# Kernel tuning notes

Hardware: AMD Instinct MI355X
Metric: run time of the kernel (lower is better)

Reference implementation:

```python
import jax, jax.numpy as jnp
import numpy as np

DIMS = [2048, 1024, 512, 256, 128, 64, 32, 16, 8, 4, 2]
IN_CH = [3, 8, 32, 64, 64, 64, 128, 256, 512, 512, 512]
FEAT = [8, 32, 64, 64, 64, 128, 256, 512, 512, 512, 1024]
B = 512
K = 16


def setup_inputs() -> dict:
    key = jax.random.key(0)
    keys = jax.random.split(key, 64)
    inp = {"x": jax.random.normal(keys[0], (B, 3, 2048), dtype=jnp.float32)}
    for i, d in enumerate(DIMS):
        inp[f"c{i}"] = jax.random.randint(keys[1 + i], (d,), 0, 3, dtype=jnp.int64)
    for i in range(11):
        cin, f = IN_CH[i], FEAT[i]
        inp[f"W{i+1}"] = jax.random.normal(keys[20 + 2 * i], (3 * f, cin), dtype=jnp.float32) / jnp.sqrt(jnp.float32(cin))
        inp[f"b{i+1}"] = jnp.zeros((3 * f,), dtype=jnp.float32)
    inp["Wfc"] = jax.random.normal(keys[60], (K, 1024), dtype=jnp.float32) / jnp.sqrt(jnp.float32(1024))
    inp["bfc"] = jnp.zeros((K,), dtype=jnp.float32)
    return inp


def _kdconv(x, W, b, sel, featdim, dim):
    # pointwise conv (kernel size 1) + relu: [B, in, dim] -> [B, 3*featdim, dim]
    y = jax.nn.relu(jnp.einsum('oi,bid->bod', W, x) + b[None, :, None])
    bsz = y.shape[0]
    # faithful to torch: view [B, featdim, 3*dim], then gather index d*3 + sel[d]
    y = y.reshape(bsz, featdim, 3 * dim)
    idx = sel + 3 * jnp.arange(dim, dtype=sel.dtype)
    y = jnp.take(y, idx, axis=2)                       # [B, featdim, dim]
    y = y.reshape(bsz, featdim, dim // 2, 2)
    return jnp.max(y, axis=-1)                          # [B, featdim, dim//2]


def reference(x, c0, c1, c2, c3, c4, c5, c6, c7, c8, c9, c10,
              W1, b1, W2, b2, W3, b3, W4, b4, W5, b5, W6, b6,
              W7, b7, W8, b8, W9, b9, W10, b10, W11, b11, Wfc, bfc):
    cs = [c0, c1, c2, c3, c4, c5, c6, c7, c8, c9, c10]
    Ws = [W1, W2, W3, W4, W5, W6, W7, W8, W9, W10, W11]
    bs = [b1, b2, b3, b4, b5, b6, b7, b8, b9, b10, b11]
    y = x
    for i in range(11):
        y = _kdconv(y, Ws[i], bs[i], cs[i], FEAT[i], DIMS[i])
    y = y.reshape(-1, 1024)
    logits = y @ Wfc.T + bfc
    return jax.nn.log_softmax(logits, axis=1)
```

## Files before the change

kernel.cpp:

```cpp
#include <hip/hip_runtime.h>
#include <cstdint>
#include <cmath>


typedef __attribute__((ext_vector_type(8))) short bhalf8;
typedef __attribute__((ext_vector_type(4))) float floatx4;

__device__ __forceinline__ unsigned short f2bf(float f) {
    uint32_t u = __float_as_uint(f);
    u += 0x7FFFu + ((u >> 16) & 1u);
    return (unsigned short)(u >> 16);
}
__device__ __forceinline__ float bf2f(unsigned short u) {
    return __uint_as_float(((uint32_t)u) << 16);
}

struct WPrep {
    const float* src[9];
    unsigned short* dst[9];
    int n4[9];
    int csh[4];
    int sm[4];
};

__global__ __launch_bounds__(256)
void l01_kernel(const float* __restrict__ x,
                const float* __restrict__ W0, const float* __restrict__ b0,
                const int* __restrict__ sel0,
                const float* __restrict__ W1, const float* __restrict__ b1,
                const int* __restrict__ sel1,
                unsigned short* __restrict__ out,
                WPrep wp, int nL1) {
    const int tid = threadIdx.x;

    if ((int)blockIdx.x >= nL1) {
        const int stride = (gridDim.x - nL1) * 256;
        const int g0 = (blockIdx.x - nL1) * 256 + tid;
        #pragma unroll
        for (int l = 0; l < 4; ++l) {
            const float4* s = reinterpret_cast<const float4*>(wp.src[l]);
            char* dbase = (char*)wp.dst[l];
            const int n16 = wp.n4[l] >> 1;
            const int csh = wp.csh[l], sm = wp.sm[l];
            for (int i = g0; i < n16; i += stride) {
                const float4 va = s[2 * i], vb = s[2 * i + 1];
                uint4 o;
                o.x = (uint32_t)f2bf(va.x) | ((uint32_t)f2bf(va.y) << 16);
                o.y = (uint32_t)f2bf(va.z) | ((uint32_t)f2bf(va.w) << 16);
                o.z = (uint32_t)f2bf(vb.x) | ((uint32_t)f2bf(vb.y) << 16);
                o.w = (uint32_t)f2bf(vb.z) | ((uint32_t)f2bf(vb.w) << 16);
                const int row = i >> csh;
                const int c   = i - (row << csh);
                *(uint4*)(dbase + (row << (csh + 4)) +
                          ((c * 16) ^ ((row & sm) << 4))) = o;
            }
        }
        #pragma unroll
        for (int l = 4; l < 9; ++l) {
            const float4* s = reinterpret_cast<const float4*>(wp.src[l]);
            uint2* d = reinterpret_cast<uint2*>(wp.dst[l]);
            for (int i = g0; i < wp.n4[l]; i += stride) {
                const float4 v = s[i];
                uint2 o;
                o.x = (uint32_t)f2bf(v.x) | ((uint32_t)f2bf(v.y) << 16);
                o.y = (uint32_t)f2bf(v.z) | ((uint32_t)f2bf(v.w) << 16);
                d[i] = o;
            }
        }
        return;
    }

    __shared__ float W0s[24][3]; __shared__ float b0s[24];
    __shared__ float W1s[96][8]; __shared__ float b1s[96];
    if (tid < 24) {
        W0s[tid][0] = W0[tid * 3 + 0];
        W0s[tid][1] = W0[tid * 3 + 1];
        W0s[tid][2] = W0[tid * 3 + 2];
        b0s[tid] = b0[tid];
    }
    if (tid < 96) {
        #pragma unroll
        for (int k = 0; k < 8; ++k) W1s[tid][k] = W1[tid * 8 + k];
        b1s[tid] = b1[tid];
    }
    __syncthreads();

    const int gid = blockIdx.x * 256 + tid;
    const int b  = gid >> 9;
    const int j1 = gid & 511;
    const float* xb = x + (size_t)b * 3 * 2048;

    float cols[2][8];
    int q1v[2];
    #pragma unroll
    for (int pos1 = 0; pos1 < 2; ++pos1) {
        const int d1 = 2 * j1 + pos1;
        const int e1 = 3 * d1 + sel1[d1];
        const int q1 = (e1 >= 1024) + (e1 >= 2048);
        const int p1 = e1 - q1 * 1024;
        q1v[pos1] = q1;

        float xv[2][3]; int qq0[2];
        #pragma unroll
        for (int pos0 = 0; pos0 < 2; ++pos0) {
            const int d0 = 2 * p1 + pos0;
            const int e0 = 3 * d0 + sel0[d0];
            const int q0 = (e0 >= 2048) + (e0 >= 4096);
            const int p0 = e0 - q0 * 2048;
            qq0[pos0] = q0;
            xv[pos0][0] = xb[p0];
            xv[pos0][1] = xb[2048 + p0];
            xv[pos0][2] = xb[4096 + p0];
        }
        #pragma unroll
        for (int f = 0; f < 8; ++f) {
            const int r0 = 3 * f + qq0[0], r1 = 3 * f + qq0[1];
            const float v0 = b0s[r0] + W0s[r0][0]*xv[0][0] + W0s[r0][1]*xv[0][1] + W0s[r0][2]*xv[0][2];
            const float v1 = b0s[r1] + W0s[r1][0]*xv[1][0] + W0s[r1][1]*xv[1][1] + W0s[r1][2]*xv[1][2];
            cols[pos1][f] = fmaxf(fmaxf(v0, v1), 0.f);
        }
    }

    unsigned short o[32];
    #pragma unroll
    for (int f = 0; f < 32; ++f) {
        const int r0 = 3 * f + q1v[0], r1 = 3 * f + q1v[1];
        float v0 = b1s[r0], v1 = b1s[r1];
        #pragma unroll
        for (int k = 0; k < 8; ++k) {
            v0 = fmaf(cols[0][k], W1s[r0][k], v0);
            v1 = fmaf(cols[1][k], W1s[r1][k], v1);
        }
        o[f] = f2bf(fmaxf(fmaxf(v0, v1), 0.f));
    }
    bhalf8* op = reinterpret_cast<bhalf8*>(out + (size_t)gid * 32);
    const int perm = j1 & 3;
    #pragma unroll
    for (int i = 0; i < 4; ++i) {
        bhalf8 v;
        #pragma unroll
        for (int k = 0; k < 8; ++k) v[k] = (short)o[8*i + k];
        op[i ^ perm] = v;
    }
}


template<int RB>
__device__ __forceinline__ int swaddr(int row, int colbyte) {
    constexpr int SM = (RB / 16 >= 8) ? 7 : (RB / 16 - 1);
    return row * RB + (colbyte ^ ((row & SM) << 4));
}

template<int DIM, int CIN, int FEAT>
__device__ __forceinline__ void kdlayer(char* pool, int offIn, int offOut,
                                        int offW, int offMisc,
                                        const unsigned short* __restrict__ Wq,
                                        const float* __restrict__ bg,
                                        const int* __restrict__ sel, int tid) {
    constexpr int NH  = CIN / 32;
    constexpr int MT  = DIM / 16;
    constexpr int NT  = FEAT / 16;
    constexpr int RBW = CIN * 2;
    constexpr int RBO = FEAT * 2;
    constexpr int WM  = (MT < 8) ? MT : 8;
    constexpr int WN  = 8 / WM;
    constexpr int MPW = MT / WM;
    constexpr int NPW = NT / WN;
    constexpr int WG16 = 3 * FEAT * CIN / 8;

    float* biasS = (float*)(pool + offMisc);
    unsigned short* qp = (unsigned short*)(pool + offMisc + 3 * FEAT * 4);

    {
        const bhalf8* src = (const bhalf8*)Wq;
        bhalf8* dst = (bhalf8*)(pool + offW);
        for (int i = tid; i < WG16; i += 512) dst[i] = src[i];
    }
    for (int i = tid; i < 3 * FEAT; i += 512) biasS[i] = bg[i];
    for (int d = tid; d < DIM; d += 512) {
        const int e = 3 * d + sel[d];
        const int q = (e >= DIM) + (e >= 2 * DIM);
        qp[d] = (unsigned short)((q << 12) | (e - q * DIM));
    }
    __syncthreads();

    const int wv = tid >> 6, ln = tid & 63;
    const int g = ln >> 4, l15 = ln & 15;
    const int wm = wv % WM, wn = wv / WM;

    bhalf8 aC[MPW][NH];
    uint32_t qpk[MPW];
    #pragma unroll
    for (int i = 0; i < MPW; ++i) {
        const int mt = wm + i * WM;
        const int pa = qp[mt * 16 + l15] & 0xFFF;
        #pragma unroll
        for (int ks = 0; ks < NH; ++ks)
            aC[i][ks] = *(const bhalf8*)(pool + offIn +
                          swaddr<RBW>(pa, (ks * 32 + g * 8) * 2));
        const ushort4 qq = *(const ushort4*)(qp + mt * 16 + g * 4);
        qpk[i] = (uint32_t)(qq.x >> 12) | ((uint32_t)(qq.y >> 12) << 4)
               | ((uint32_t)(qq.z >> 12) << 8) | ((uint32_t)(qq.w >> 12) << 12);
    }

    #pragma unroll
    for (int ntj = 0; ntj < NPW; ++ntj) {
        const int nt = wn * NPW + ntj;
        const int f = nt * 16 + l15;
        bhalf8 bF[3][NH];
        #pragma unroll
        for (int q = 0; q < 3; ++q)
            #pragma unroll
            for (int ks = 0; ks < NH; ++ks)
                bF[q][ks] = *(const bhalf8*)(pool + offW +
                              swaddr<RBW>(3 * f + q, (ks * 32 + g * 8) * 2));
        #pragma unroll
        for (int i = 0; i < MPW; ++i) {
            floatx4 a0 = (floatx4){0.f,0.f,0.f,0.f};
            floatx4 a1 = (floatx4){0.f,0.f,0.f,0.f};
            floatx4 a2 = (floatx4){0.f,0.f,0.f,0.f};
            #pragma unroll
            for (int ks = 0; ks < NH; ++ks) {
                a0 = __builtin_amdgcn_mfma_f32_16x16x32_bf16(aC[i][ks], bF[0][ks], a0, 0, 0, 0);
                a1 = __builtin_amdgcn_mfma_f32_16x16x32_bf16(aC[i][ks], bF[1][ks], a1, 0, 0, 0);
                a2 = __builtin_amdgcn_mfma_f32_16x16x32_bf16(aC[i][ks], bF[2][ks], a2, 0, 0, 0);
            }
            const int mt = wm + i * WM;
            const int j0 = mt * 8 + g * 2;
            float v[4];
            #pragma unroll
            for (int r = 0; r < 4; ++r) {
                const int qi = (qpk[i] >> (4 * r)) & 0xF;
                const float pre = (qi == 0) ? a0[r] : (qi == 1 ? a1[r] : a2[r]);
                v[r] = pre + biasS[3 * f + qi];
            }
            *(unsigned short*)(pool + offOut + swaddr<RBO>(j0,     f * 2)) =
                f2bf(fmaxf(fmaxf(v[0], v[1]), 0.f));
            *(unsigned short*)(pool + offOut + swaddr<RBO>(j0 + 1, f * 2)) =
                f2bf(fmaxf(fmaxf(v[2], v[3]), 0.f));
        }
    }
    __syncthreads();
}

__global__ __launch_bounds__(512)
void chain_kernel(const unsigned short* __restrict__ act,
                  unsigned short* __restrict__ out,
                  const unsigned short* __restrict__ w2, const float* __restrict__ b2, const int* __restrict__ s2,
                  const unsigned short* __restrict__ w3, const float* __restrict__ b3, const int* __restrict__ s3,
                  const unsigned short* __restrict__ w4, const float* __restrict__ b4, const int* __restrict__ s4,
                  const unsigned short* __restrict__ w5, const float* __restrict__ b5, const int* __restrict__ s5) {
    __shared__ __align__(16) char pool[79872];
    const int tid = threadIdx.x;
    const int b = blockIdx.x;

    {
        const bhalf8* src = (const bhalf8*)(act + (size_t)b * 512 * 32);
        bhalf8* dst = (bhalf8*)pool;
        #pragma unroll
        for (int k = 0; k < 4; ++k) dst[k * 512 + tid] = src[k * 512 + tid];
    }

    kdlayer<512, 32,  64>(pool, 0,     47104, 32768, 45056, w2, b2, s2, tid);
    kdlayer<256, 64,  64>(pool, 47104, 0,     16384, 40960, w3, b3, s3, tid);
    kdlayer<128, 64,  64>(pool, 0,     16384, 24576, 49152, w4, b4, s4, tid);
    kdlayer< 64, 64, 128>(pool, 16384, 0,     24576, 73728, w5, b5, s5, tid);

    {
        char* dst = (char*)(out + (size_t)b * 32 * 128);
        const int off = tid * 16;
        const bhalf8 v = *(const bhalf8*)(pool + swaddr<256>(off >> 8, off & 255));
        *(bhalf8*)(dst + off) = v;
    }
}

template<int CIN, int BT>
__global__ __launch_bounds__(256)
void kdmfma_kernel(const unsigned short* __restrict__ act,
                   const unsigned short* __restrict__ Wq,
                   const float* __restrict__ bias,
                   const int*   __restrict__ sel,
                   unsigned short* __restrict__ out,
                   int feat, int dim, int nbt) {
    constexpr int KS  = (CIN >= 128) ? 128 : CIN;
    constexpr int NH  = KS / 32;
    constexpr int LDK = KS + 8;
    constexpr int TPA = 256 / BT;
    constexpr int EA  = KS / TPA;
    constexpr int NSA = EA / 8;
    constexpr int NSW = KS / 32;
    constexpr int MF  = 2;
    constexpr int NF  = (BT == 64) ? 2 : 1;
    __shared__ __align__(16) unsigned short Ab[BT][LDK];
    __shared__ __align__(16) unsigned short Wb[64][LDK];

    const int dimh = dim >> 1;
    const int bt = blockIdx.x % nbt;
    const int j  = blockIdx.x / nbt;
    const int f0 = blockIdx.y * 64;
    const int b0 = bt * BT;

    const int tid  = threadIdx.x;
    const int lane = tid & 63;
    const int wave = tid >> 6;

    const int srowA = tid / TPA;
    const int kgA   = (tid % TPA) * EA;
    const int srowW = tid >> 2;
    const int kgW   = (tid & 3) * (KS / 4);

    const int rowBase = (BT == 64) ? (wave & 1) * 32 : 0;
    const int colBase = (BT == 64) ? (wave >> 1) * 32 : wave * 16;

    floatx4 acc[2][MF][NF];
    #pragma unroll
    for (int pp = 0; pp < 2; ++pp)
        #pragma unroll
        for (int mi = 0; mi < MF; ++mi)
            #pragma unroll
            for (int ni = 0; ni < NF; ++ni)
                acc[pp][mi][ni] = (floatx4){0.f, 0.f, 0.f, 0.f};
    int qv[2];

    #pragma unroll
    for (int pp = 0; pp < 2; ++pp) {
        const int d = 2 * j + pp;
        const int s = sel[d];
        const int e = 3 * d + s;
        const int q = (e >= dim) + (e >= 2 * dim);
        const int p = e - q * dim;
        qv[pp] = q;

        const unsigned short* Ap = act + ((size_t)(b0 + srowA) * dim + p) * CIN + kgA;
        const unsigned short* Wp = Wq + ((size_t)(3 * (f0 + srowW) + q)) * CIN + kgW;

        bhalf8 pa[NSA], pw[NSW];
        #pragma unroll
        for (int u = 0; u < NSA; ++u)
            pa[u] = *reinterpret_cast<const bhalf8*>(Ap + u * 8);
        #pragma unroll
        for (int u = 0; u < NSW; ++u)
            pw[u] = *reinterpret_cast<const bhalf8*>(Wp + u * 8);

        for (int k0 = 0; k0 < CIN; k0 += KS) {
            __syncthreads();
            #pragma unroll
            for (int u = 0; u < NSA; ++u)
                *reinterpret_cast<bhalf8*>(&Ab[srowA][kgA + u * 8]) = pa[u];
            #pragma unroll
            for (int u = 0; u < NSW; ++u)
                *reinterpret_cast<bhalf8*>(&Wb[srowW][kgW + u * 8]) = pw[u];
            if (k0 + KS < CIN) {
                #pragma unroll
                for (int u = 0; u < NSA; ++u)
                    pa[u] = *reinterpret_cast<const bhalf8*>(Ap + k0 + KS + u * 8);
                #pragma unroll
                for (int u = 0; u < NSW; ++u)
                    pw[u] = *reinterpret_cast<const bhalf8*>(Wp + k0 + KS + u * 8);
            }
            __syncthreads();

            #pragma unroll
            for (int ks = 0; ks < NH; ++ks) {
                const int kk = ks * 32 + (lane >> 4) * 8;
                bhalf8 aF[MF], bF[NF];
                #pragma unroll
                for (int mi = 0; mi < MF; ++mi)
                    aF[mi] = *reinterpret_cast<const bhalf8*>(
                        &Ab[rowBase + mi * 16 + (lane & 15)][kk]);
                #pragma unroll
                for (int ni = 0; ni < NF; ++ni)
                    bF[ni] = *reinterpret_cast<const bhalf8*>(
                        &Wb[colBase + ni * 16 + (lane & 15)][kk]);
                #pragma unroll
                for (int mi = 0; mi < MF; ++mi)
                    #pragma unroll
                    for (int ni = 0; ni < NF; ++ni)
                        acc[pp][mi][ni] = __builtin_amdgcn_mfma_f32_16x16x32_bf16(
                            aF[mi], bF[ni], acc[pp][mi][ni], 0, 0, 0);
            }
        }
    }

    const int orow = (lane >> 4) << 2;
    const int ocol = lane & 15;
    #pragma unroll
    for (int mi = 0; mi < MF; ++mi)
        #pragma unroll
        for (int ni = 0; ni < NF; ++ni) {
            const int fc = f0 + colBase + ni * 16 + ocol;
            const float bv0 = bias[3 * fc + qv[0]];
            const float bv1 = bias[3 * fc + qv[1]];
            #pragma unroll
            for (int i = 0; i < 4; ++i) {
                const int br = b0 + rowBase + mi * 16 + orow + i;
                const float v = fmaxf(fmaxf(acc[0][mi][ni][i] + bv0,
                                            acc[1][mi][ni][i] + bv1), 0.f);
                out[((size_t)br * dimh + j) * feat + fc] = f2bf(v);
            }
        }
}

__global__ __launch_bounds__(256)
void fc_lsm_kernel(const unsigned short* __restrict__ y,
                   const float* __restrict__ Wfc,
                   const float* __restrict__ bfc,
                   float* __restrict__ out) {
    const int b   = blockIdx.x;
    const int tid = threadIdx.x;
    __shared__ __align__(16) float ys[1024];
    __shared__ float lg[16];

    {
        const ushort4 v = reinterpret_cast<const ushort4*>(y + (size_t)b * 1024)[tid];
        ys[tid * 4 + 0] = bf2f(v.x);
        ys[tid * 4 + 1] = bf2f(v.y);
        ys[tid * 4 + 2] = bf2f(v.z);
        ys[tid * 4 + 3] = bf2f(v.w);
    }
    __syncthreads();

    const int l = tid >> 4, lane = tid & 15;
    const float4* w4 = reinterpret_cast<const float4*>(Wfc + (size_t)l * 1024);
    const float4* y4 = reinterpret_cast<const float4*>(ys);
    float p = 0.f;
    #pragma unroll
    for (int i = 0; i < 16; ++i) {
        const float4 a = y4[lane + 16 * i];
        const float4 w = w4[lane + 16 * i];
        p += a.x * w.x + a.y * w.y + a.z * w.z + a.w * w.w;
    }
    #pragma unroll
    for (int off = 8; off > 0; off >>= 1) p += __shfl_down(p, off, 16);
    if (lane == 0) lg[l] = p + bfc[l];
    __syncthreads();

    if (tid < 16) {
        float m = -1e30f;
        #pragma unroll
        for (int i = 0; i < 16; ++i) m = fmaxf(m, lg[i]);
        float s = 0.f;
        #pragma unroll
        for (int i = 0; i < 16; ++i) s += expf(lg[i] - m);
        out[b * 16 + tid] = lg[tid] - m - logf(s);
    }
}

extern "C" void kernel_launch(void* const* d_in, const int* in_sizes, int n_in,
                              void* d_out, int out_size, void* d_ws, size_t ws_size,
                              hipStream_t stream) {
    static const int LFEAT[11] = {8, 32, 64, 64, 64, 128, 256, 512, 512, 512, 1024};
    static const int LDIM[11]  = {2048, 1024, 512, 256, 128, 64, 32, 16, 8, 4, 2};
    static const int LCIN[11]  = {3, 8, 32, 64, 64, 64, 128, 256, 512, 512, 512};

    const float* x = (const float*)d_in[0];
    const int B = in_sizes[0] / (3 * 2048);

    const size_t slot = (size_t)B * 32 * 512;
    float* bufA = (float*)d_ws;
    float* bufB = bufA + slot;
    unsigned short* wq = (unsigned short*)(bufB + slot);

    const float* W[11]; const float* bi[11]; const int* sl[11];
    for (int i = 0; i < 11; ++i) {
        W[i]  = (const float*)d_in[12 + 2 * i];
        bi[i] = (const float*)d_in[13 + 2 * i];
        sl[i] = (const int*)d_in[1 + i];
    }

    unsigned short* wqp[11];
    {
        size_t off = 0;
        for (int i = 2; i <= 10; ++i) {
            wqp[i] = wq + off;
            off += (size_t)3 * LFEAT[i] * LCIN[i];
        }
    }

    unsigned short* actA = (unsigned short*)bufA;
    unsigned short* actB = (unsigned short*)bufB;

    {
        WPrep wp;
        for (int i = 2; i <= 10; ++i) {
            wp.src[i - 2] = W[i];
            wp.dst[i - 2] = wqp[i];
            wp.n4[i - 2]  = (3 * LFEAT[i] * LCIN[i]) / 4;
        }
        static const int CSH[4] = {2, 3, 3, 3};
        static const int SMV[4] = {3, 7, 7, 7};
        for (int l = 0; l < 4; ++l) { wp.csh[l] = CSH[l]; wp.sm[l] = SMV[l]; }
        const int nL1 = (B * 512) / 256;
        l01_kernel<<<nL1 + 768, 256, 0, stream>>>(x, W[0], bi[0], sl[0],
                                                  W[1], bi[1], sl[1],
                                                  actB, wp, nL1);
    }

    chain_kernel<<<B, 512, 0, stream>>>(actB, actA,
                                        wqp[2], bi[2], sl[2],
                                        wqp[3], bi[3], sl[3],
                                        wqp[4], bi[4], sl[4],
                                        wqp[5], bi[5], sl[5]);

    const int nbt64 = B / 64;
    const int nbt32 = B / 32;

    {   dim3 g((LDIM[6]/2) * nbt64, LFEAT[6]/64);
        kdmfma_kernel<128, 64><<<g, 256, 0, stream>>>(actA, wqp[6], bi[6], sl[6], actB, LFEAT[6], LDIM[6], nbt64); }
    {   dim3 g((LDIM[7]/2) * nbt64, LFEAT[7]/64);
        kdmfma_kernel<256, 64><<<g, 256, 0, stream>>>(actB, wqp[7], bi[7], sl[7], actA, LFEAT[7], LDIM[7], nbt64); }

    {   dim3 g((LDIM[8]/2) * nbt32, LFEAT[8]/64);
        kdmfma_kernel<512, 32><<<g, 256, 0, stream>>>(actA, wqp[8], bi[8], sl[8], actB, LFEAT[8], LDIM[8], nbt32); }
    {   dim3 g((LDIM[9]/2) * nbt32, LFEAT[9]/64);
        kdmfma_kernel<512, 32><<<g, 256, 0, stream>>>(actB, wqp[9], bi[9], sl[9], actA, LFEAT[9], LDIM[9], nbt32); }
    {   dim3 g((LDIM[10]/2) * nbt32, LFEAT[10]/64);
        kdmfma_kernel<512, 32><<<g, 256, 0, stream>>>(actA, wqp[10], bi[10], sl[10], actB, LFEAT[10], LDIM[10], nbt32); }

    fc_lsm_kernel<<<B, 256, 0, stream>>>(actB, (const float*)d_in[34],
                                         (const float*)d_in[35], (float*)d_out);
}
```

Baseline: 102.5 us.

## Read chain-layer weights and first-layer input directly from global, shrink LDS pool

The chain kernel no longer stages per-layer weights, bias and the layer-2 input activations into shared memory. B fragments and bias come straight from global memory (L2-resident linear bf16 weights), and layer 2 reads its gathered A rows directly from global. All gather-index tables are precomputed once up front, and the LDS pool drops from about 78KB to 50KB with a launch-bounds occupancy hint of 6. The weight-prep path no longer writes swizzled layouts. This removes the per-layer copy-then-barrier phases and lets more blocks fit per CU, at the cost of uncoalesced, repeated global and L2 reads of weights across waves and blocks.

```diff
diff --git a/kernel.cpp b/kernel.cpp
--- a/kernel.cpp
+++ b/kernel.cpp
@@ -19,8 +19,6 @@
     const float* src[9];
     unsigned short* dst[9];
     int n4[9];
-    int csh[4];
-    int sm[4];
 };
 
 __global__ __launch_bounds__(256)
@@ -37,26 +35,7 @@
         const int stride = (gridDim.x - nL1) * 256;
         const int g0 = (blockIdx.x - nL1) * 256 + tid;
         #pragma unroll
-        for (int l = 0; l < 4; ++l) {
-            const float4* s = reinterpret_cast<const float4*>(wp.src[l]);
-            char* dbase = (char*)wp.dst[l];
-            const int n16 = wp.n4[l] >> 1;
-            const int csh = wp.csh[l], sm = wp.sm[l];
-            for (int i = g0; i < n16; i += stride) {
-                const float4 va = s[2 * i], vb = s[2 * i + 1];
-                uint4 o;
-                o.x = (uint32_t)f2bf(va.x) | ((uint32_t)f2bf(va.y) << 16);
-                o.y = (uint32_t)f2bf(va.z) | ((uint32_t)f2bf(va.w) << 16);
-                o.z = (uint32_t)f2bf(vb.x) | ((uint32_t)f2bf(vb.y) << 16);
-                o.w = (uint32_t)f2bf(vb.z) | ((uint32_t)f2bf(vb.w) << 16);
-                const int row = i >> csh;
-                const int c   = i - (row << csh);
-                *(uint4*)(dbase + (row << (csh + 4)) +
-                          ((c * 16) ^ ((row & sm) << 4))) = o;
-            }
-        }
-        #pragma unroll
-        for (int l = 4; l < 9; ++l) {
+        for (int l = 0; l < 9; ++l) {
             const float4* s = reinterpret_cast<const float4*>(wp.src[l]);
             uint2* d = reinterpret_cast<uint2*>(wp.dst[l]);
             for (int i = g0; i < wp.n4[l]; i += stride) {
@@ -134,13 +113,12 @@
         o[f] = f2bf(fmaxf(fmaxf(v0, v1), 0.f));
     }
     bhalf8* op = reinterpret_cast<bhalf8*>(out + (size_t)gid * 32);
-    const int perm = j1 & 3;
     #pragma unroll
     for (int i = 0; i < 4; ++i) {
         bhalf8 v;
         #pragma unroll
         for (int k = 0; k < 8; ++k) v[k] = (short)o[8*i + k];
-        op[i ^ perm] = v;
+        op[i] = v;
     }
 }
 
@@ -151,12 +129,12 @@
     return row * RB + (colbyte ^ ((row & SM) << 4));
 }
 
-template<int DIM, int CIN, int FEAT>
-__device__ __forceinline__ void kdlayer(char* pool, int offIn, int offOut,
-                                        int offW, int offMisc,
-                                        const unsigned short* __restrict__ Wq,
+template<int DIM, int CIN, int FEAT, bool GA>
+__device__ __forceinline__ void kdlayer(char* pool, const unsigned short* gA,
+                                        int offIn, int offOut, int qpOff,
+                                        const unsigned short* __restrict__ wlin,
                                         const float* __restrict__ bg,
-                                        const int* __restrict__ sel, int tid) {
+                                        int tid) {
     constexpr int NH  = CIN / 32;
     constexpr int MT  = DIM / 16;
     constexpr int NT  = FEAT / 16;
@@ -166,24 +144,8 @@
     constexpr int WN  = 8 / WM;
     constexpr int MPW = MT / WM;
     constexpr int NPW = NT / WN;
-    constexpr int WG16 = 3 * FEAT * CIN / 8;
-
-    float* biasS = (float*)(pool + offMisc);
-    unsigned short* qp = (unsigned short*)(pool + offMisc + 3 * FEAT * 4);
-
-    {
-        const bhalf8* src = (const bhalf8*)Wq;
-        bhalf8* dst = (bhalf8*)(pool + offW);
-        for (int i = tid; i < WG16; i += 512) dst[i] = src[i];
-    }
-    for (int i = tid; i < 3 * FEAT; i += 512) biasS[i] = bg[i];
-    for (int d = tid; d < DIM; d += 512) {
-        const int e = 3 * d + sel[d];
-        const int q = (e >= DIM) + (e >= 2 * DIM);
-        qp[d] = (unsigned short)((q << 12) | (e - q * DIM));
-    }
-    __syncthreads();
-
+
+    const unsigned short* qp = (const unsigned short*)(pool + qpOff);
     const int wv = tid >> 6, ln = tid & 63;
     const int g = ln >> 4, l15 = ln & 15;
     const int wm = wv % WM, wn = wv / WM;
@@ -195,9 +157,13 @@
         const int mt = wm + i * WM;
         const int pa = qp[mt * 16 + l15] & 0xFFF;
         #pragma unroll
-        for (int ks = 0; ks < NH; ++ks)
-            aC[i][ks] = *(const bhalf8*)(pool + offIn +
-                          swaddr<RBW>(pa, (ks * 32 + g * 8) * 2));
+        for (int ks = 0; ks < NH; ++ks) {
+            if constexpr (GA)
+                aC[i][ks] = *(const bhalf8*)(gA + (size_t)pa * CIN + ks * 32 + g * 8);
+            else
+                aC[i][ks] = *(const bhalf8*)(pool + offIn +
+                              swaddr<RBW>(pa, (ks * 32 + g * 8) * 2));
+        }
         const ushort4 qq = *(const ushort4*)(qp + mt * 16 + g * 4);
         qpk[i] = (uint32_t)(qq.x >> 12) | ((uint32_t)(qq.y >> 12) << 4)
                | ((uint32_t)(qq.z >> 12) << 8) | ((uint32_t)(qq.w >> 12) << 12);
@@ -212,8 +178,11 @@
         for (int q = 0; q < 3; ++q)
             #pragma unroll
             for (int ks = 0; ks < NH; ++ks)
-                bF[q][ks] = *(const bhalf8*)(pool + offW +
-                              swaddr<RBW>(3 * f + q, (ks * 32 + g * 8) * 2));
+                bF[q][ks] = *(const bhalf8*)(wlin + (size_t)(3 * f + q) * CIN
+                                             + ks * 32 + g * 8);
+        const float bv0 = bg[3 * f + 0];
+        const float bv1 = bg[3 * f + 1];
+        const float bv2 = bg[3 * f + 2];
         #pragma unroll
         for (int i = 0; i < MPW; ++i) {
             floatx4 a0 = (floatx4){0.f,0.f,0.f,0.f};
@@ -232,7 +201,8 @@
             for (int r = 0; r < 4; ++r) {
                 const int qi = (qpk[i] >> (4 * r)) & 0xF;
                 const float pre = (qi == 0) ? a0[r] : (qi == 1 ? a1[r] : a2[r]);
-                v[r] = pre + biasS[3 * f + qi];
+                const float bq  = (qi == 0) ? bv0  : (qi == 1 ? bv1  : bv2);
+                v[r] = pre + bq;
             }
             *(unsigned short*)(pool + offOut + swaddr<RBO>(j0,     f * 2)) =
                 f2bf(fmaxf(fmaxf(v[0], v[1]), 0.f));
@@ -240,36 +210,58 @@
                 f2bf(fmaxf(fmaxf(v[2], v[3]), 0.f));
         }
     }
-    __syncthreads();
-}
-
-__global__ __launch_bounds__(512)
+}
+
+__global__ __launch_bounds__(512, 6)
 void chain_kernel(const unsigned short* __restrict__ act,
                   unsigned short* __restrict__ out,
                   const unsigned short* __restrict__ w2, const float* __restrict__ b2, const int* __restrict__ s2,
                   const unsigned short* __restrict__ w3, const float* __restrict__ b3, const int* __restrict__ s3,
                   const unsigned short* __restrict__ w4, const float* __restrict__ b4, const int* __restrict__ s4,
                   const unsigned short* __restrict__ w5, const float* __restrict__ b5, const int* __restrict__ s5) {
-    __shared__ __align__(16) char pool[79872];
+    __shared__ __align__(16) char pool[51200];
     const int tid = threadIdx.x;
     const int b = blockIdx.x;
 
     {
-        const bhalf8* src = (const bhalf8*)(act + (size_t)b * 512 * 32);
-        bhalf8* dst = (bhalf8*)pool;
-        #pragma unroll
-        for (int k = 0; k < 4; ++k) dst[k * 512 + tid] = src[k * 512 + tid];
-    }
-
-    kdlayer<512, 32,  64>(pool, 0,     47104, 32768, 45056, w2, b2, s2, tid);
-    kdlayer<256, 64,  64>(pool, 47104, 0,     16384, 40960, w3, b3, s3, tid);
-    kdlayer<128, 64,  64>(pool, 0,     16384, 24576, 49152, w4, b4, s4, tid);
-    kdlayer< 64, 64, 128>(pool, 16384, 0,     24576, 73728, w5, b5, s5, tid);
+        unsigned short* qp2 = (unsigned short*)(pool + 0);
+        unsigned short* qp3 = (unsigned short*)(pool + 1024);
+        unsigned short* qp4 = (unsigned short*)(pool + 1536);
+        unsigned short* qp5 = (unsigned short*)(pool + 1792);
+        { const int d = tid;
+          const int e = 3 * d + s2[d];
+          const int q = (e >= 512) + (e >= 1024);
+          qp2[d] = (unsigned short)((q << 12) | (e - q * 512)); }
+        if (tid < 256) { const int d = tid;
+          const int e = 3 * d + s3[d];
+          const int q = (e >= 256) + (e >= 512);
+          qp3[d] = (unsigned short)((q << 12) | (e - q * 256)); }
+        if (tid < 128) { const int d = tid;
+          const int e = 3 * d + s4[d];
+          const int q = (e >= 128) + (e >= 256);
+          qp4[d] = (unsigned short)((q << 12) | (e - q * 128)); }
+        if (tid < 64)  { const int d = tid;
+          const int e = 3 * d + s5[d];
+          const int q = (e >= 64) + (e >= 128);
+          qp5[d] = (unsigned short)((q << 12) | (e - q * 64)); }
+    }
+    __syncthreads();
+
+    kdlayer<512, 32,  64, true >(pool, act + (size_t)b * 512 * 32,
+                                 0,     2048,  0,    w2, b2, tid);
+    __syncthreads();
+    kdlayer<256, 64,  64, false>(pool, nullptr, 2048,  34816, 1024, w3, b3, tid);
+    __syncthreads();
+    kdlayer<128, 64,  64, false>(pool, nullptr, 34816, 2048,  1536, w4, b4, tid);
+    __syncthreads();
+    kdlayer< 64, 64, 128, false>(pool, nullptr, 2048,  10240, 1792, w5, b5, tid);
+    __syncthreads();
 
     {
         char* dst = (char*)(out + (size_t)b * 32 * 128);
         const int off = tid * 16;
-        const bhalf8 v = *(const bhalf8*)(pool + swaddr<256>(off >> 8, off & 255));
+        const bhalf8 v = *(const bhalf8*)(pool + 10240 +
+                                          swaddr<256>(off >> 8, off & 255));
         *(bhalf8*)(dst + off) = v;
     }
 }
@@ -487,9 +479,6 @@
             wp.dst[i - 2] = wqp[i];
             wp.n4[i - 2]  = (3 * LFEAT[i] * LCIN[i]) / 4;
         }
-        static const int CSH[4] = {2, 3, 3, 3};
-        static const int SMV[4] = {3, 7, 7, 7};
-        for (int l = 0; l < 4; ++l) { wp.csh[l] = CSH[l]; wp.sm[l] = SMV[l]; }
         const int nL1 = (B * 512) / 256;
         l01_kernel<<<nL1 + 768, 256, 0, stream>>>(x, W[0], bi[0], sl[0],
                                                   W[1], bi[1], sl[1],
```

Measured after the change: 111.3 us. 1.09x slower.
